# Optimization experiments

Hardware: AMD Instinct MI355X
Metric: run time of the kernel (lower is better)

Reference implementation:

```python
import jax, jax.numpy as jnp
import numpy as np

TEMPERATURE = 0.07
EPS = 1e-12  # F.normalize eps


def setup_inputs() -> dict:
    key = jax.random.key(0)
    k1, k2, k3 = jax.random.split(key, 3)
    B, D, N_CLASSES = 4096, 256, 1000
    return {
        "z_i": jax.random.normal(k1, (B, D), dtype=jnp.float32),
        "z_j": jax.random.normal(k2, (B, D), dtype=jnp.float32),
        "labels": jax.random.randint(k3, (B,), 0, N_CLASSES, dtype=jnp.int64),
    }


def _l2_normalize(x):
    norm = jnp.sqrt(jnp.sum(x * x, axis=1, keepdims=True))
    return x / jnp.maximum(norm, EPS)


def reference(z_i, z_j, labels):
    zi = _l2_normalize(z_i)
    zj = _l2_normalize(z_j)
    z = jnp.concatenate([zi, zj], axis=0)          # (2B, D)
    lab = jnp.concatenate([labels, labels], axis=0)  # (2B,)
    N = z.shape[0]

    sim = jnp.matmul(z, z.T) / TEMPERATURE          # (2B, 2B)

    eye = jnp.eye(N, dtype=bool)
    same = lab[:, None] == lab[None, :]
    pos_mask = same & ~eye                          # positives: same label, not self
    neg_mask = ~same                                # negatives: different label

    # pos_sim_i = sum of similarities over positives (a sum, per original code)
    pos_sim = jnp.sum(jnp.where(pos_mask, sim, 0.0), axis=1)  # (2B,)
    # log(neg_sim_i) = logsumexp over negatives (stable, same math as sum of exp)
    lse_neg = jax.nn.logsumexp(jnp.where(neg_mask, sim, -jnp.inf), axis=1)
    # -log(exp(p) / (exp(p) + n)) = log(1 + exp(log n - p))
    loss_i = jnp.logaddexp(0.0, lse_neg - pos_sim)  # (2B,)

    has_pos = jnp.any(pos_mask, axis=1)
    loss = jnp.sum(jnp.where(has_pos, loss_i, 0.0)) / N
    return loss
```

## Files before the change

### kernel.cpp

```cpp
#include <hip/hip_runtime.h>

#define NROWS 8192
#define BQ    4096
#define DDIM  256
#define INV_T (1.0f/0.07f)
#define K2EXP (1.4426950408889634f/0.07f)

typedef short bf16x8 __attribute__((ext_vector_type(8)));
typedef float f32x4  __attribute__((ext_vector_type(4)));
typedef unsigned short u16;

__device__ __forceinline__ u16 f2bf(float f) {
  unsigned u = __float_as_uint(f);
  u += 0x7fffu + ((u >> 16) & 1u);
  return (u16)(u >> 16);
}

__global__ void norm_cast_kernel(const float* __restrict__ zi,
                                 const float* __restrict__ zj,
                                 u16* __restrict__ zb,
                                 float* __restrict__ posneg,
                                 float* __restrict__ out) {
  if (blockIdx.x == 0 && threadIdx.x == 0) *out = 0.0f;
  if (blockIdx.x < 64) posneg[blockIdx.x * 256 + threadIdx.x] = 0.0f;
  int wave = threadIdx.x >> 6;
  int lane = threadIdx.x & 63;
  int row  = blockIdx.x * 4 + wave;
  const float* src = (row < BQ) ? (zi + (size_t)row * DDIM)
                                : (zj + (size_t)(row - BQ) * DDIM);
  float4 v = ((const float4*)src)[lane];
  float s = v.x*v.x + v.y*v.y + v.z*v.z + v.w*v.w;
  #pragma unroll
  for (int m = 32; m; m >>= 1) s += __shfl_xor(s, m, 64);
  float scale = 1.0f / fmaxf(sqrtf(s), 1e-12f);
  ushort4 o;
  o.x = f2bf(v.x * scale); o.y = f2bf(v.y * scale);
  o.z = f2bf(v.z * scale); o.w = f2bf(v.w * scale);
  ((ushort4*)(zb + (size_t)row * DDIM))[lane] = o;
}

#define GL2LDS(gp, lp) \
  __builtin_amdgcn_global_load_lds((__attribute__((address_space(1))) void*)(gp), \
                                   (__attribute__((address_space(3))) void*)(lp), 16, 0, 0)

__global__ __launch_bounds__(256) void simloss_kernel(
    const u16* __restrict__ zb, const int* __restrict__ labels,
    float* __restrict__ pos, float* __restrict__ neg) {
  __shared__ __align__(16) u16 lsA[128 * 32];
  __shared__ __align__(16) u16 lsB[128 * 32];

  const int tid  = threadIdx.x;
  const int w    = tid >> 6;
  const int lane = tid & 63;
  const int ln   = lane & 15;
  const int qd   = lane >> 4;
  const int wr   = w >> 1;
  const int wc   = w & 1;

  const int u = blockIdx.x;
  int rb = (int)((129.0f - sqrtf((float)(16641 - 8 * u))) * 0.5f);
  while ((rb + 1) * (129 - (rb + 1)) / 2 <= u) ++rb;
  while (rb * (129 - rb) / 2 > u) --rb;
  const int cbk = rb + (u - rb * (129 - rb) / 2);
  const int r0 = rb * 128;
  const int c0 = cbk * 128;

  const int strow = lane >> 2;
  const int slot  = lane & 3;
  const int stk   = (slot ^ ((strow >> 1) & 3)) * 8;
  const int rdsw  = (ln >> 1) & 3;

  int rowidx[16], rowlab[16];
  #pragma unroll
  for (int ri = 0; ri < 4; ++ri)
    #pragma unroll
    for (int r = 0; r < 4; ++r) {
      int slt = ri * 4 + r;
      int row = r0 + wr * 64 + ri * 16 + qd * 4 + r;
      rowidx[slt] = row;
      rowlab[slt] = labels[row & (BQ - 1)];
    }
  int colv[4], clab[4];
  #pragma unroll
  for (int mi = 0; mi < 4; ++mi) {
    colv[mi] = c0 + wc * 64 + mi * 16 + ln;
    clab[mi] = labels[colv[mi] & (BQ - 1)];
  }

  const f32x4 z4 = {0.f, 0.f, 0.f, 0.f};
  f32x4 acc[4][4];
  #pragma unroll
  for (int ri = 0; ri < 4; ++ri)
    #pragma unroll
    for (int mi = 0; mi < 4; ++mi) acc[ri][mi] = z4;

  for (int kk = 0; kk < 8; ++kk) {
    const int k0 = kk * 32;
    #pragma unroll
    for (int j = 0; j < 2; ++j) {
      int rbase = w * 32 + j * 16;
      const u16* ga = zb + (size_t)(r0 + rbase + strow) * DDIM + k0 + stk;
      GL2LDS(ga, &lsA[rbase * 32]);
      const u16* gb = zb + (size_t)(c0 + rbase + strow) * DDIM + k0 + stk;
      GL2LDS(gb, &lsB[rbase * 32]);
    }
    __syncthreads();

    bf16x8 av[4], bv[4];
    #pragma unroll
    for (int ri = 0; ri < 4; ++ri)
      av[ri] = *(const bf16x8*)&lsA[(wr * 64 + ri * 16 + ln) * 32 + (qd ^ rdsw) * 8];
    #pragma unroll
    for (int mi = 0; mi < 4; ++mi)
      bv[mi] = *(const bf16x8*)&lsB[(wc * 64 + mi * 16 + ln) * 32 + (qd ^ rdsw) * 8];
    #pragma unroll
    for (int ri = 0; ri < 4; ++ri)
      #pragma unroll
      for (int mi = 0; mi < 4; ++mi)
        acc[ri][mi] = __builtin_amdgcn_mfma_f32_16x16x32_bf16(
            av[ri], bv[mi], acc[ri][mi], 0, 0, 0);
    __syncthreads();
  }

  float posA[16], negA[16];
  #pragma unroll
  for (int i = 0; i < 16; ++i) { posA[i] = 0.0f; negA[i] = 0.0f; }

  if (rb == cbk) {
    #pragma unroll
    for (int ri = 0; ri < 4; ++ri)
      #pragma unroll
      for (int mi = 0; mi < 4; ++mi) {
        f32x4 v = acc[ri][mi];
        #pragma unroll
        for (int r = 0; r < 4; ++r) {
          int slt = ri * 4 + r;
          float s = v[r];
          bool same = (rowlab[slt] == clab[mi]);
          bool diag = (rowidx[slt] == colv[mi]);
          posA[slt] += (same && !diag) ? s : 0.0f;
          negA[slt] += same ? 0.0f : __builtin_amdgcn_exp2f(s * K2EXP);
        }
      }
  } else {
    float cpos[4], cneg[4];
    #pragma unroll
    for (int mi = 0; mi < 4; ++mi) { cpos[mi] = 0.0f; cneg[mi] = 0.0f; }
    #pragma unroll
    for (int ri = 0; ri < 4; ++ri)
      #pragma unroll
      for (int mi = 0; mi < 4; ++mi) {
        f32x4 v = acc[ri][mi];
        #pragma unroll
        for (int r = 0; r < 4; ++r) {
          int slt = ri * 4 + r;
          float s = v[r];
          bool same = (rowlab[slt] == clab[mi]);
          float e = same ? 0.0f : __builtin_amdgcn_exp2f(s * K2EXP);
          float p = same ? s : 0.0f;
          posA[slt] += p;  negA[slt] += e;
          cpos[mi]  += p;  cneg[mi]  += e;
        }
      }
    #pragma unroll
    for (int mi = 0; mi < 4; ++mi) {
      cpos[mi] += __shfl_xor(cpos[mi], 16, 64);
      cpos[mi] += __shfl_xor(cpos[mi], 32, 64);
      cneg[mi] += __shfl_xor(cneg[mi], 16, 64);
      cneg[mi] += __shfl_xor(cneg[mi], 32, 64);
    }
    if (qd == 0) {
      #pragma unroll
      for (int mi = 0; mi < 4; ++mi) {
        atomicAdd(&pos[colv[mi]], cpos[mi]);
        atomicAdd(&neg[colv[mi]], cneg[mi]);
      }
    }
  }

  #pragma unroll
  for (int i = 0; i < 16; ++i) {
    #pragma unroll
    for (int m = 1; m < 16; m <<= 1) {
      posA[i] += __shfl_xor(posA[i], m, 64);
      negA[i] += __shfl_xor(negA[i], m, 64);
    }
  }
  if (ln == 0) {
    #pragma unroll
    for (int i = 0; i < 16; ++i) {
      atomicAdd(&pos[rowidx[i]], posA[i]);
      atomicAdd(&neg[rowidx[i]], negA[i]);
    }
  }
}

__global__ void loss_kernel(const float* __restrict__ pos,
                            const float* __restrict__ neg,
                            float* __restrict__ out) {
  int row = blockIdx.x * 256 + threadIdx.x;
  float p = pos[row];
  float n = neg[row];
  float l = log1pf(expf(logf(n) - p * INV_T));
  #pragma unroll
  for (int m = 32; m; m >>= 1) l += __shfl_xor(l, m, 64);
  __shared__ float red[4];
  if ((threadIdx.x & 63) == 0) red[threadIdx.x >> 6] = l;
  __syncthreads();
  if (threadIdx.x == 0) {
    float tot = red[0] + red[1] + red[2] + red[3];
    atomicAdd(out, tot * (1.0f / NROWS));
  }
}

extern "C" void kernel_launch(void* const* d_in, const int* in_sizes, int n_in,
                              void* d_out, int out_size, void* d_ws, size_t ws_size,
                              hipStream_t stream) {
  const float* zi     = (const float*)d_in[0];
  const float* zj     = (const float*)d_in[1];
  const int*   labels = (const int*)d_in[2];
  float*       out    = (float*)d_out;

  char* w = (char*)d_ws;
  u16*   zb  = (u16*)w;
  float* pos = (float*)(w + (size_t)NROWS * DDIM * sizeof(u16));
  float* neg = pos + NROWS;

  hipLaunchKernelGGL(norm_cast_kernel, dim3(2048), dim3(256), 0, stream,
                     zi, zj, zb, pos, out);
  hipLaunchKernelGGL(simloss_kernel, dim3(2080), dim3(256), 0, stream,
                     zb, labels, pos, neg);
  hipLaunchKernelGGL(loss_kernel, dim3(32), dim3(256), 0, stream,
                     pos, neg, out);
}
```

Measured before the change: 141.0 us.

## Replace atomics with per-slice partial buffers and group column tiles per block

Each block now owns one row tile and up to four consecutive column tiles of the upper triangle, in a 64x16 grid with early exit. It accumulates row sums across those tiles in registers. Row and column partials are written with plain stores into 160 disjoint slices instead of being added atomically to shared pos/neg arrays. The final loss kernel sums the 160 slices per row. This removes atomic contention and cuts the number of row-sum writes, but it adds zeroing of a large partial buffer in the norm kernel, a heavier reduction pass, and some blocks exiting early or doing uneven work.

```diff
diff --git a/kernel.cpp b/kernel.cpp
--- a/kernel.cpp
+++ b/kernel.cpp
@@ -3,6 +3,7 @@
 #define NROWS 8192
 #define BQ    4096
 #define DDIM  256
+#define NSLC  160
 #define INV_T (1.0f/0.07f)
 #define K2EXP (1.4426950408889634f/0.07f)
 
@@ -19,10 +20,15 @@
 __global__ void norm_cast_kernel(const float* __restrict__ zi,
                                  const float* __restrict__ zj,
                                  u16* __restrict__ zb,
-                                 float* __restrict__ posneg,
+                                 float* __restrict__ partials,
                                  float* __restrict__ out) {
   if (blockIdx.x == 0 && threadIdx.x == 0) *out = 0.0f;
-  if (blockIdx.x < 64) posneg[blockIdx.x * 256 + threadIdx.x] = 0.0f;
+  {
+    unsigned gid = blockIdx.x * 256 + threadIdx.x;
+    #pragma unroll
+    for (int i = 0; i < 5; ++i)
+      partials[(size_t)i * 524288 + gid] = 0.0f;
+  }
   int wave = threadIdx.x >> 6;
   int lane = threadIdx.x & 63;
   int row  = blockIdx.x * 4 + wave;
@@ -45,9 +51,13 @@
 
 __global__ __launch_bounds__(256) void simloss_kernel(
     const u16* __restrict__ zb, const int* __restrict__ labels,
-    float* __restrict__ pos, float* __restrict__ neg) {
+    float* __restrict__ pos_p, float* __restrict__ neg_p) {
   __shared__ __align__(16) u16 lsA[128 * 32];
   __shared__ __align__(16) u16 lsB[128 * 32];
+
+  const int rb = blockIdx.x;
+  const int g  = blockIdx.y;
+  if (4 * g + 3 < rb) return;
 
   const int tid  = threadIdx.x;
   const int w    = tid >> 6;
@@ -56,14 +66,7 @@
   const int qd   = lane >> 4;
   const int wr   = w >> 1;
   const int wc   = w & 1;
-
-  const int u = blockIdx.x;
-  int rb = (int)((129.0f - sqrtf((float)(16641 - 8 * u))) * 0.5f);
-  while ((rb + 1) * (129 - (rb + 1)) / 2 <= u) ++rb;
-  while (rb * (129 - rb) / 2 > u) --rb;
-  const int cbk = rb + (u - rb * (129 - rb) / 2);
-  const int r0 = rb * 128;
-  const int c0 = cbk * 128;
+  const int r0   = rb * 128;
 
   const int strow = lane >> 2;
   const int slot  = lane & 3;
@@ -80,100 +83,107 @@
       rowidx[slt] = row;
       rowlab[slt] = labels[row & (BQ - 1)];
     }
-  int colv[4], clab[4];
-  #pragma unroll
-  for (int mi = 0; mi < 4; ++mi) {
-    colv[mi] = c0 + wc * 64 + mi * 16 + ln;
-    clab[mi] = labels[colv[mi] & (BQ - 1)];
-  }
-
-  const f32x4 z4 = {0.f, 0.f, 0.f, 0.f};
-  f32x4 acc[4][4];
-  #pragma unroll
-  for (int ri = 0; ri < 4; ++ri)
-    #pragma unroll
-    for (int mi = 0; mi < 4; ++mi) acc[ri][mi] = z4;
-
-  for (int kk = 0; kk < 8; ++kk) {
-    const int k0 = kk * 32;
-    #pragma unroll
-    for (int j = 0; j < 2; ++j) {
-      int rbase = w * 32 + j * 16;
-      const u16* ga = zb + (size_t)(r0 + rbase + strow) * DDIM + k0 + stk;
-      GL2LDS(ga, &lsA[rbase * 32]);
-      const u16* gb = zb + (size_t)(c0 + rbase + strow) * DDIM + k0 + stk;
-      GL2LDS(gb, &lsB[rbase * 32]);
-    }
-    __syncthreads();
-
-    bf16x8 av[4], bv[4];
+
+  float posA[16], negA[16];
+  #pragma unroll
+  for (int i = 0; i < 16; ++i) { posA[i] = 0.0f; negA[i] = 0.0f; }
+
+  for (int ci = 0; ci < 4; ++ci) {
+    const int c = 4 * g + ci;
+    if (c < rb) continue;
+    const int c0 = c * 128;
+    int colv[4], clab[4];
+    #pragma unroll
+    for (int mi = 0; mi < 4; ++mi) {
+      colv[mi] = c0 + wc * 64 + mi * 16 + ln;
+      clab[mi] = labels[colv[mi] & (BQ - 1)];
+    }
+
+    const f32x4 z4 = {0.f, 0.f, 0.f, 0.f};
+    f32x4 acc[4][4];
     #pragma unroll
     for (int ri = 0; ri < 4; ++ri)
-      av[ri] = *(const bf16x8*)&lsA[(wr * 64 + ri * 16 + ln) * 32 + (qd ^ rdsw) * 8];
-    #pragma unroll
-    for (int mi = 0; mi < 4; ++mi)
-      bv[mi] = *(const bf16x8*)&lsB[(wc * 64 + mi * 16 + ln) * 32 + (qd ^ rdsw) * 8];
-    #pragma unroll
-    for (int ri = 0; ri < 4; ++ri)
+      #pragma unroll
+      for (int mi = 0; mi < 4; ++mi) acc[ri][mi] = z4;
+
+    for (int kk = 0; kk < 8; ++kk) {
+      const int k0 = kk * 32;
+      #pragma unroll
+      for (int j = 0; j < 2; ++j) {
+        int rbase = w * 32 + j * 16;
+        const u16* ga = zb + (size_t)(r0 + rbase + strow) * DDIM + k0 + stk;
+        GL2LDS(ga, &lsA[rbase * 32]);
+        const u16* gb = zb + (size_t)(c0 + rbase + strow) * DDIM + k0 + stk;
+        GL2LDS(gb, &lsB[rbase * 32]);
+      }
+      __syncthreads();
+
+      bf16x8 av[4], bv[4];
+      #pragma unroll
+      for (int ri = 0; ri < 4; ++ri)
+        av[ri] = *(const bf16x8*)&lsA[(wr * 64 + ri * 16 + ln) * 32 + (qd ^ rdsw) * 8];
       #pragma unroll
       for (int mi = 0; mi < 4; ++mi)
-        acc[ri][mi] = __builtin_amdgcn_mfma_f32_16x16x32_bf16(
-            av[ri], bv[mi], acc[ri][mi], 0, 0, 0);
-    __syncthreads();
-  }
-
-  float posA[16], negA[16];
-  #pragma unroll
-  for (int i = 0; i < 16; ++i) { posA[i] = 0.0f; negA[i] = 0.0f; }
-
-  if (rb == cbk) {
-    #pragma unroll
-    for (int ri = 0; ri < 4; ++ri)
+        bv[mi] = *(const bf16x8*)&lsB[(wc * 64 + mi * 16 + ln) * 32 + (qd ^ rdsw) * 8];
+      #pragma unroll
+      for (int ri = 0; ri < 4; ++ri)
+        #pragma unroll
+        for (int mi = 0; mi < 4; ++mi)
+          acc[ri][mi] = __builtin_amdgcn_mfma_f32_16x16x32_bf16(
+              av[ri], bv[mi], acc[ri][mi], 0, 0, 0);
+      __syncthreads();
+    }
+
+    if (c == rb) {
+      #pragma unroll
+      for (int ri = 0; ri < 4; ++ri)
+        #pragma unroll
+        for (int mi = 0; mi < 4; ++mi) {
+          f32x4 v = acc[ri][mi];
+          #pragma unroll
+          for (int r = 0; r < 4; ++r) {
+            int slt = ri * 4 + r;
+            float s = v[r];
+            bool same = (rowlab[slt] == clab[mi]);
+            bool diag = (rowidx[slt] == colv[mi]);
+            posA[slt] += (same && !diag) ? s : 0.0f;
+            negA[slt] += same ? 0.0f : __builtin_amdgcn_exp2f(s * K2EXP);
+          }
+        }
+    } else {
+      float cpos[4], cneg[4];
+      #pragma unroll
+      for (int mi = 0; mi < 4; ++mi) { cpos[mi] = 0.0f; cneg[mi] = 0.0f; }
+      #pragma unroll
+      for (int ri = 0; ri < 4; ++ri)
+        #pragma unroll
+        for (int mi = 0; mi < 4; ++mi) {
+          f32x4 v = acc[ri][mi];
+          #pragma unroll
+          for (int r = 0; r < 4; ++r) {
+            int slt = ri * 4 + r;
+            float s = v[r];
+            bool same = (rowlab[slt] == clab[mi]);
+            float e = same ? 0.0f : __builtin_amdgcn_exp2f(s * K2EXP);
+            float p = same ? s : 0.0f;
+            posA[slt] += p;  negA[slt] += e;
+            cpos[mi]  += p;  cneg[mi]  += e;
+          }
+        }
       #pragma unroll
       for (int mi = 0; mi < 4; ++mi) {
-        f32x4 v = acc[ri][mi];
-        #pragma unroll
-        for (int r = 0; r < 4; ++r) {
-          int slt = ri * 4 + r;
-          float s = v[r];
-          bool same = (rowlab[slt] == clab[mi]);
-          bool diag = (rowidx[slt] == colv[mi]);
-          posA[slt] += (same && !diag) ? s : 0.0f;
-          negA[slt] += same ? 0.0f : __builtin_amdgcn_exp2f(s * K2EXP);
+        cpos[mi] += __shfl_xor(cpos[mi], 16, 64);
+        cpos[mi] += __shfl_xor(cpos[mi], 32, 64);
+        cneg[mi] += __shfl_xor(cneg[mi], 16, 64);
+        cneg[mi] += __shfl_xor(cneg[mi], 32, 64);
+      }
+      if (qd == 0) {
+        const size_t scs = (size_t)(32 + 2 * rb + wr) * NROWS;
+        #pragma unroll
+        for (int mi = 0; mi < 4; ++mi) {
+          pos_p[scs + colv[mi]] = cpos[mi];
+          neg_p[scs + colv[mi]] = cneg[mi];
         }
-      }
-  } else {
-    float cpos[4], cneg[4];
-    #pragma unroll
-    for (int mi = 0; mi < 4; ++mi) { cpos[mi] = 0.0f; cneg[mi] = 0.0f; }
-    #pragma unroll
-    for (int ri = 0; ri < 4; ++ri)
-      #pragma unroll
-      for (int mi = 0; mi < 4; ++mi) {
-        f32x4 v = acc[ri][mi];
-        #pragma unroll
-        for (int r = 0; r < 4; ++r) {
-          int slt = ri * 4 + r;
-          float s = v[r];
-          bool same = (rowlab[slt] == clab[mi]);
-          float e = same ? 0.0f : __builtin_amdgcn_exp2f(s * K2EXP);
-          float p = same ? s : 0.0f;
-          posA[slt] += p;  negA[slt] += e;
-          cpos[mi]  += p;  cneg[mi]  += e;
-        }
-      }
-    #pragma unroll
-    for (int mi = 0; mi < 4; ++mi) {
-      cpos[mi] += __shfl_xor(cpos[mi], 16, 64);
-      cpos[mi] += __shfl_xor(cpos[mi], 32, 64);
-      cneg[mi] += __shfl_xor(cneg[mi], 16, 64);
-      cneg[mi] += __shfl_xor(cneg[mi], 32, 64);
-    }
-    if (qd == 0) {
-      #pragma unroll
-      for (int mi = 0; mi < 4; ++mi) {
-        atomicAdd(&pos[colv[mi]], cpos[mi]);
-        atomicAdd(&neg[colv[mi]], cneg[mi]);
       }
     }
   }
@@ -187,30 +197,29 @@
     }
   }
   if (ln == 0) {
+    const size_t srs = (size_t)(2 * g + wc) * NROWS;
     #pragma unroll
     for (int i = 0; i < 16; ++i) {
-      atomicAdd(&pos[rowidx[i]], posA[i]);
-      atomicAdd(&neg[rowidx[i]], negA[i]);
-    }
-  }
-}
-
-__global__ void loss_kernel(const float* __restrict__ pos,
-                            const float* __restrict__ neg,
+      pos_p[srs + rowidx[i]] = posA[i];
+      neg_p[srs + rowidx[i]] = negA[i];
+    }
+  }
+}
+
+__global__ void loss_kernel(const float* __restrict__ pos_p,
+                            const float* __restrict__ neg_p,
                             float* __restrict__ out) {
-  int row = blockIdx.x * 256 + threadIdx.x;
-  float p = pos[row];
-  float n = neg[row];
+  int row = blockIdx.x * 64 + threadIdx.x;
+  float p = 0.0f, n = 0.0f;
+  #pragma unroll 8
+  for (int s = 0; s < NSLC; ++s) {
+    p += pos_p[(size_t)s * NROWS + row];
+    n += neg_p[(size_t)s * NROWS + row];
+  }
   float l = log1pf(expf(logf(n) - p * INV_T));
   #pragma unroll
   for (int m = 32; m; m >>= 1) l += __shfl_xor(l, m, 64);
-  __shared__ float red[4];
-  if ((threadIdx.x & 63) == 0) red[threadIdx.x >> 6] = l;
-  __syncthreads();
-  if (threadIdx.x == 0) {
-    float tot = red[0] + red[1] + red[2] + red[3];
-    atomicAdd(out, tot * (1.0f / NROWS));
-  }
+  if (threadIdx.x == 0) atomicAdd(out, l * (1.0f / NROWS));
 }
 
 extern "C" void kernel_launch(void* const* d_in, const int* in_sizes, int n_in,
@@ -222,14 +231,14 @@
   float*       out    = (float*)d_out;
 
   char* w = (char*)d_ws;
-  u16*   zb  = (u16*)w;
-  float* pos = (float*)(w + (size_t)NROWS * DDIM * sizeof(u16));
-  float* neg = pos + NROWS;
+  u16*   zb    = (u16*)w;
+  float* pos_p = (float*)(w + (size_t)NROWS * DDIM * sizeof(u16));
+  float* neg_p = pos_p + (size_t)NSLC * NROWS;
 
   hipLaunchKernelGGL(norm_cast_kernel, dim3(2048), dim3(256), 0, stream,
-                     zi, zj, zb, pos, out);
-  hipLaunchKernelGGL(simloss_kernel, dim3(2080), dim3(256), 0, stream,
-                     zb, labels, pos, neg);
-  hipLaunchKernelGGL(loss_kernel, dim3(32), dim3(256), 0, stream,
-                     pos, neg, out);
-}
+                     zi, zj, zb, pos_p, out);
+  hipLaunchKernelGGL(simloss_kernel, dim3(64, 16), dim3(256), 0, stream,
+                     zb, labels, pos_p, neg_p);
+  hipLaunchKernelGGL(loss_kernel, dim3(128), dim3(64), 0, stream,
+                     pos_p, neg_p, out);
+}
```

New measurement: 159.5 us. +13.2%, slower.
